# Kernel tuning notes

Measured on AMD Instinct MI355X. Metric: run time of the kernel, lower is better.

The kernel has to match this reference:

```python
import jax, jax.numpy as jnp
import numpy as np

B, NA, NB = 2, 2048, 2048
DIM_A, DIM_B = 256, 256
HEADS, DH_A, DH_B = 8, 64, 64
INNER_A, INNER_B = DH_A * HEADS, DH_B * HEADS
EPS = 1e-5


def layer_norm(x, w, b):
    m = jnp.mean(x, axis=-1, keepdims=True)
    v = jnp.mean(jnp.square(x - m), axis=-1, keepdims=True)
    return (x - m) * jax.lax.rsqrt(v + EPS) * w + b


def setup_inputs() -> dict:
    key = jax.random.key(0)
    ks = jax.random.split(key, 16)
    s = 0.02
    return {
        "feat_a": jax.random.normal(ks[0], (B, NA, DIM_A), jnp.float32),
        "feat_b": jax.random.normal(ks[1], (B, NB, DIM_B), jnp.float32),
        "mask_a_b": jax.random.bernoulli(ks[2], 0.5, (B, NA, NB)),
        # linear weights stored (in, out)
        "Wq": jax.random.normal(ks[3], (DIM_A, INNER_B), jnp.float32) * s,
        "bq": jnp.zeros((INNER_B,), jnp.float32),
        "Wk": jax.random.normal(ks[4], (DIM_B, INNER_B), jnp.float32) * s,
        "bk": jnp.zeros((INNER_B,), jnp.float32),
        "Wv": jax.random.normal(ks[5], (DIM_B, INNER_A), jnp.float32) * s,
        "bv": jnp.zeros((INNER_A,), jnp.float32),
        "Wg": jax.random.normal(ks[6], (DIM_A, INNER_A), jnp.float32) * s,
        "bg": jnp.zeros((INNER_A,), jnp.float32),
        "Wo": jax.random.normal(ks[7], (INNER_A, DIM_A), jnp.float32) * s,
        "bo": jnp.zeros((DIM_A,), jnp.float32),
        "ln_a_w": jnp.ones((DIM_A,), jnp.float32),
        "ln_a_b": jnp.zeros((DIM_A,), jnp.float32),
        "ln_b_w": jnp.ones((DIM_B,), jnp.float32),
        "ln_b_b": jnp.zeros((DIM_B,), jnp.float32),
        "qln_w": jnp.ones((INNER_B,), jnp.float32),
        "qln_b": jnp.zeros((INNER_B,), jnp.float32),
        "kln_w": jnp.ones((INNER_B,), jnp.float32),
        "kln_b": jnp.zeros((INNER_B,), jnp.float32),
    }


def reference(feat_a, feat_b, mask_a_b, Wq, bq, Wk, bk, Wv, bv, Wg, bg, Wo, bo,
              ln_a_w, ln_a_b, ln_b_w, ln_b_b, qln_w, qln_b, kln_w, kln_b):
    scale = DH_B ** -0.5
    fa = layer_norm(feat_a, ln_a_w, ln_a_b)            # (b, na, dim_a)
    fb = layer_norm(feat_b, ln_b_w, ln_b_b)            # (b, nb, dim_b)
    q = layer_norm(fa @ Wq + bq, qln_w, qln_b)         # (b, na, inner_b)
    k = layer_norm(fb @ Wk + bk, kln_w, kln_b)         # (b, nb, inner_b)
    v = fb @ Wv + bv                                   # (b, nb, inner_a)
    g = fa @ Wg + bg                                   # (b, na, inner_a)
    q = q.reshape(B, NA, HEADS, DH_B)
    k = k.reshape(B, NB, HEADS, DH_B)
    v = v.reshape(B, NB, HEADS, DH_A)
    g = g.reshape(B, NA, HEADS, DH_A)
    sim = jnp.einsum('bihd,bjhd->bhij', q, k) * scale  # (b, h, na, nb)
    neg = jnp.finfo(sim.dtype).min
    sim = jnp.where(mask_a_b[:, None, :, :], sim, neg)
    attn = jax.nn.softmax(sim, axis=-1)
    out = jnp.einsum('bhij,bjhd->bihd', attn, v)       # (b, na, h, dh_a)
    out = jax.nn.sigmoid(g) * out
    out = out.reshape(B, NA, INNER_A)
    return out @ Wo + bo                               # (b, na, dim_a)
```

## Files before the change

### kernel.cpp

```cpp
#include <hip/hip_runtime.h>
#include <hip/hip_bf16.h>

using bf16 = __hip_bfloat16;
typedef short bf16x8 __attribute__((ext_vector_type(8)));
typedef float f32x4 __attribute__((ext_vector_type(4)));
typedef unsigned short ushort8_t __attribute__((ext_vector_type(8)));
typedef unsigned long long u64;

static constexpr int NA_ = 2048, NB_ = 2048;
static constexpr int H_ = 8, DH_ = 64, INNER_ = 512;
static constexpr int MROWS = 2 * NA_;

#define MFMA32(a, b, c) __builtin_amdgcn_mfma_f32_16x16x32_bf16(a, b, c, 0, 0, 0)

#if __has_builtin(__builtin_amdgcn_exp2f)
#define EXP2(x) __builtin_amdgcn_exp2f(x)
#else
#define EXP2(x) exp2f(x)
#endif

__device__ __forceinline__ unsigned short bfbits(float x) {
  bf16 h = __float2bfloat16(x);
  return __builtin_bit_cast(unsigned short, h);
}
__device__ __forceinline__ float b2f(unsigned short u) {
  unsigned v = ((unsigned)u) << 16;
  return __builtin_bit_cast(float, v);
}

__device__ __forceinline__ unsigned pkbf(float a, float b) {
  unsigned ua = __builtin_bit_cast(unsigned, a) + 0x8000u;
  unsigned ub = __builtin_bit_cast(unsigned, b) + 0x8000u;
#if __has_builtin(__builtin_amdgcn_perm)
  return __builtin_amdgcn_perm(ub, ua, 0x07060302u);
#else
  return (ua >> 16) | (ub & 0xFFFF0000u);
#endif
}

__global__ __launch_bounds__(256) void prep_kernel(
    const float* __restrict__ fa_in, const float* __restrict__ fb_in,
    const float* __restrict__ law, const float* __restrict__ lab,
    const float* __restrict__ lbw, const float* __restrict__ lbb,
    bf16* __restrict__ fa, bf16* __restrict__ fb,
    const float* __restrict__ Wq, const float* __restrict__ Wk,
    const float* __restrict__ Wv, const float* __restrict__ Wg,
    const float* __restrict__ Wo,
    bf16* __restrict__ Wqt, bf16* __restrict__ Wkt,
    bf16* __restrict__ Wvt, bf16* __restrict__ Wgt,
    bf16* __restrict__ Woth, bf16* __restrict__ Wotl,
    const void* __restrict__ maskp, u64* __restrict__ mbits) {
  int blk = blockIdx.x;
  int t = threadIdx.x;
  if (blk < 2048) {
    int row = blk * 4 + (t >> 6);
    int lane = t & 63;
    const float *src, *w, *bb;
    bf16* dst;
    int r;
    if (row < MROWS) { src = fa_in; w = law; bb = lab; dst = fa; r = row; }
    else             { src = fb_in; w = lbw; bb = lbb; dst = fb; r = row - MROWS; }
    float4 x = *(const float4*)(src + (size_t)r * 256 + lane * 4);
    float s  = (x.x + x.y) + (x.z + x.w);
    float s2 = (x.x * x.x + x.y * x.y) + (x.z * x.z + x.w * x.w);
#pragma unroll
    for (int m = 32; m >= 1; m >>= 1) { s += __shfl_xor(s, m); s2 += __shfl_xor(s2, m); }
    float mean = s * (1.0f / 256.0f);
    float var  = s2 * (1.0f / 256.0f) - mean * mean;
    float rstd = rsqrtf(var + 1e-5f);
    float4 wv = *(const float4*)(w + lane * 4);
    float4 bv = *(const float4*)(bb + lane * 4);
    ushort4 o;
    o.x = bfbits((x.x - mean) * rstd * wv.x + bv.x);
    o.y = bfbits((x.y - mean) * rstd * wv.y + bv.y);
    o.z = bfbits((x.z - mean) * rstd * wv.z + bv.z);
    o.w = bfbits((x.w - mean) * rstd * wv.w + bv.w);
    *(ushort4*)(dst + (size_t)r * 256 + lane * 4) = o;
  } else if (blk < 4608) {
    int z = (blk - 2048) >> 9;
    int idx = ((blk - 2048) & 511) * 256 + t;
    if (z < 4) {
      const float* W = (z == 0) ? Wq : (z == 1) ? Wk : (z == 2) ? Wv : Wg;
      bf16* Wt = (z == 0) ? Wqt : (z == 1) ? Wkt : (z == 2) ? Wvt : Wgt;
      int kk = idx >> 9, n = idx & 511;
      Wt[n * 256 + kk] = __float2bfloat16(W[idx]);
    } else {
      int kk = idx >> 8, n = idx & 255;
      float w = Wo[idx];
      bf16 hi = __float2bfloat16(w);
      Woth[n * 512 + kk] = hi;
      Wotl[n * 512 + kk] = __float2bfloat16(w - __bfloat162float(hi));
    }
  } else {
    __shared__ unsigned shf[4];
    const unsigned char* mu = (const unsigned char*)maskp;
    bool nz = ((t & 3) != 0) && (mu[t] != 0);
    u64 bal = __ballot(nz);
    if ((t & 63) == 0) shf[t >> 6] = (bal != 0ull) ? 1u : 0u;
    __syncthreads();
    bool m8 = (shf[0] | shf[1] | shf[2] | shf[3]) != 0;
    int lane = t & 63, wid = t >> 6;
    int lb = blk - 4608;
    for (size_t word = (size_t)lb * 4 + wid; word < 131072; word += 8192) {
      size_t e = word * 64 + lane;
      int v = m8 ? (int)mu[e] : ((const int*)maskp)[e];
      u64 b2 = __ballot(v != 0);
      if (lane == 0) mbits[word] = b2;
    }
  }
}

__global__ __launch_bounds__(256) void gemm4_kernel(
    const bf16* __restrict__ fa, const bf16* __restrict__ fb,
    const bf16* __restrict__ Wqt, const bf16* __restrict__ Wkt,
    const bf16* __restrict__ Wgt, const bf16* __restrict__ Wvt,
    const float* __restrict__ bq, const float* __restrict__ bk,
    const float* __restrict__ bg, const float* __restrict__ bv,
    const float* __restrict__ qlw, const float* __restrict__ qlb,
    const float* __restrict__ klw, const float* __restrict__ klb,
    bf16* __restrict__ qo, bf16* __restrict__ ko,
    bf16* __restrict__ gout, bf16* __restrict__ vout) {
  __shared__ __align__(16) char sm[27648];
  int z = blockIdx.z;
  int t = threadIdx.x, wave = t >> 6, lane = t & 63;
  int lm = lane & 15, quad = lane >> 4, q8 = quad * 8;

  if (z < 2) {
    bf16* As = (bf16*)sm;
    float* Pred = (float*)(sm + 16896);
    float* MV   = (float*)(sm + 17408);
    const bf16* A    = z ? fb : fa;
    const bf16* Wt   = z ? Wkt : Wqt;
    const float* bias = z ? bk : bq;
    const float* lw  = z ? klw : qlw;
    const float* lb  = z ? klb : qlb;
    bf16* out        = z ? ko : qo;
    int m0 = blockIdx.x * 16;
#pragma unroll
    for (int i = 0; i < 2; i++) {
      int id = t + 256 * i, r = id >> 5, cg = id & 31;
      *(ushort8_t*)(&As[r * 264 + cg * 8]) =
          *(const ushort8_t*)(A + (size_t)(m0 + r) * 256 + cg * 8);
    }
    __syncthreads();
    int n0w = wave * 128;
    f32x4 acc[8] = {};
    const bf16* wrow[8];
#pragma unroll
    for (int ni = 0; ni < 8; ni++) wrow[ni] = Wt + (size_t)(n0w + ni * 16 + lm) * 256;
#pragma unroll
    for (int ks = 0; ks < 8; ks++) {
      int k0 = ks * 32;
      bf16x8 af = *(const bf16x8*)(&As[lm * 264 + k0 + q8]);
#pragma unroll
      for (int ni = 0; ni < 8; ni++) {
        bf16x8 bf_ = *(const bf16x8*)(wrow[ni] + k0 + q8);
        acc[ni] = MFMA32(af, bf_, acc[ni]);
      }
    }
    float bvv[8];
#pragma unroll
    for (int ni = 0; ni < 8; ni++) bvv[ni] = bias[n0w + ni * 16 + lm];
#pragma unroll
    for (int ni = 0; ni < 8; ni++)
#pragma unroll
      for (int r = 0; r < 4; r++) acc[ni][r] += bvv[ni];
#pragma unroll
    for (int r = 0; r < 4; r++) {
      float s = 0.f, s2 = 0.f;
#pragma unroll
      for (int ni = 0; ni < 8; ni++) { s += acc[ni][r]; s2 += acc[ni][r] * acc[ni][r]; }
#pragma unroll
      for (int m = 1; m <= 8; m <<= 1) { s += __shfl_xor(s, m); s2 += __shfl_xor(s2, m); }
      if (lm == 0) {
        int row = quad * 4 + r;
        Pred[row * 8 + wave * 2]     = s;
        Pred[row * 8 + wave * 2 + 1] = s2;
      }
    }
    __syncthreads();
    if (t < 16) {
      float s = 0.f, s2 = 0.f;
#pragma unroll
      for (int w = 0; w < 4; w++) { s += Pred[t * 8 + w * 2]; s2 += Pred[t * 8 + w * 2 + 1]; }
      float mean = s * (1.0f / 512.0f);
      float var  = s2 * (1.0f / 512.0f) - mean * mean;
      MV[t * 2]     = mean;
      MV[t * 2 + 1] = rsqrtf(var + 1e-5f);
    }
    __syncthreads();
    float lww[8], lbb_[8];
#pragma unroll
    for (int ni = 0; ni < 8; ni++) {
      lww[ni]  = lw[n0w + ni * 16 + lm];
      lbb_[ni] = lb[n0w + ni * 16 + lm];
    }
    if (z == 0) {
      const float SC = 0.125f * 1.44269504088896f;
#pragma unroll
      for (int ni = 0; ni < 8; ni++) { lww[ni] *= SC; lbb_[ni] *= SC; }
    }
#pragma unroll
    for (int r = 0; r < 4; r++) {
      int row = quad * 4 + r;
      float mean = MV[row * 2], rstd = MV[row * 2 + 1];
      size_t obase = (size_t)(m0 + row) * 512 + n0w;
#pragma unroll
      for (int ni = 0; ni < 8; ni++)
        out[obase + ni * 16 + lm] =
            __float2bfloat16((acc[ni][r] - mean) * rstd * lww[ni] + lbb_[ni]);
    }
  } else {
    bf16* As = (bf16*)sm;
    bf16* Bs = (bf16*)(sm + 18432);
    const bf16* A    = (z == 3) ? fb : fa;
    const bf16* Wt   = (z == 3) ? Wvt : Wgt;
    const float* bias = (z == 3) ? bv : bg;
    int x = blockIdx.x;
    int m0 = (x >> 3) * 128, n0 = (x & 7) * 64;
    int wm = wave * 32;
    f32x4 acc[2][4] = {};
    for (int k0 = 0; k0 < 256; k0 += 64) {
      __syncthreads();
#pragma unroll
      for (int i = 0; i < 4; i++) {
        int id = t + 256 * i, r = id >> 3, cg = id & 7;
        *(ushort8_t*)(&As[r * 72 + cg * 8]) =
            *(const ushort8_t*)(A + (size_t)(m0 + r) * 256 + k0 + cg * 8);
      }
#pragma unroll
      for (int i = 0; i < 2; i++) {
        int id = t + 256 * i, r = id >> 3, cg = id & 7;
        *(ushort8_t*)(&Bs[r * 72 + cg * 8]) =
            *(const ushort8_t*)(Wt + (size_t)(n0 + r) * 256 + k0 + cg * 8);
      }
      __syncthreads();
#pragma unroll
      for (int kk = 0; kk < 64; kk += 32) {
        bf16x8 af[2], bf_[4];
#pragma unroll
        for (int mi = 0; mi < 2; mi++)
          af[mi] = *(const bf16x8*)(&As[(wm + mi * 16 + lm) * 72 + kk + q8]);
#pragma unroll
        for (int ni = 0; ni < 4; ni++)
          bf_[ni] = *(const bf16x8*)(&Bs[(ni * 16 + lm) * 72 + kk + q8]);
#pragma unroll
        for (int mi = 0; mi < 2; mi++)
#pragma unroll
          for (int ni = 0; ni < 4; ni++)
            acc[mi][ni] = MFMA32(af[mi], bf_[ni], acc[mi][ni]);
      }
    }
    if (z == 2) {
#pragma unroll
      for (int mi = 0; mi < 2; mi++)
#pragma unroll
        for (int ni = 0; ni < 4; ni++) {
          int nn = n0 + ni * 16 + lm;
          float bvv = bias[nn];
          int mb = m0 + wm + mi * 16 + quad * 4;
#pragma unroll
          for (int r = 0; r < 4; r++)
            gout[(size_t)(mb + r) * 512 + nn] = __float2bfloat16(acc[mi][ni][r] + bvv);
        }
    } else {
      __syncthreads();
      bf16* buf = (bf16*)sm;
#pragma unroll
      for (int mi = 0; mi < 2; mi++)
#pragma unroll
        for (int ni = 0; ni < 4; ni++) {
          int d_local = ni * 16 + lm;
          float bvv = bias[n0 + d_local];
          int j_local = wm + mi * 16 + quad * 4;
#pragma unroll
          for (int r = 0; r < 4; r++)
            buf[d_local * 136 + j_local + r] = __float2bfloat16(acc[mi][ni][r] + bvv);
        }
      __syncthreads();
      int bidx2 = m0 >> 11, j0g = m0 & 2047, hh = n0 >> 6;
      int dl = t >> 2, jseg = (t & 3) * 32;
      bf16* dstrow = vout + (size_t)((bidx2 * 8 + hh) * 64 + dl) * 2048 + j0g + jseg;
#pragma unroll
      for (int c = 0; c < 4; c++)
        *(ushort8_t*)(dstrow + c * 8) = *(const ushort8_t*)(&buf[dl * 136 + jseg + c * 8]);
    }
  }
}

__global__ __launch_bounds__(512) void attn_kernel(
    const bf16* __restrict__ q, const bf16* __restrict__ k,
    const bf16* __restrict__ vt, const bf16* __restrict__ g,
    const u64* __restrict__ mbits,
    bf16* __restrict__ gh, bf16* __restrict__ gl) {
  __shared__ __align__(16) char smem[65024];
  bf16* Qs = (bf16*)smem;
  bf16* KsB = (bf16*)(smem + 9216);
  bf16* VsB = (bf16*)(smem + 27648);
  bf16* PsB = (bf16*)(smem + 46080);
  float* Om = (float*)(smem + 9216);
  float* Lbuf = (float*)(smem + 64512);

  int qt = blockIdx.x, bh = blockIdx.y;
  int bidx = bh >> 3, h = bh & 7;
  int i0 = qt * 64;
  int t = threadIdx.x, wave = t >> 6, lane = t & 63;
  int jhalf = wave >> 2, w4 = wave & 3;
  int lm = lane & 15, quad = lane >> 4, q8 = quad * 8;
  int lt = t & 255;
  int sr0 = lt >> 3, scg = (lt & 7) * 8;

  {
    int r = t >> 3, cg = t & 7;
    *(ushort8_t*)(&Qs[r * 72 + cg * 8]) =
        *(const ushort8_t*)(q + (size_t)(bidx * NA_ + i0 + r) * INNER_ + h * DH_ + cg * 8);
  }
  __syncthreads();
  bf16x8 bq0 = *(const bf16x8*)(&Qs[(w4 * 16 + lm) * 72 + q8]);
  bf16x8 bq1 = *(const bf16x8*)(&Qs[(w4 * 16 + lm) * 72 + 32 + q8]);

  bf16x8 bone;
  {
    short onev = (lm == 0) ? (short)0x3F80 : (short)0;
#pragma unroll
    for (int i = 0; i < 8; i++) bone[i] = onev;
  }

  f32x4 oacc[4] = {};
  f32x4 lacc = {};

  const bf16* kb = k + (size_t)(bidx * NB_) * INNER_ + h * DH_;
  const bf16* vb = vt + (size_t)(bh * DH_) * NB_;
  bf16* Pw = PsB + wave * (16 * 72);
  bf16* Ks = KsB + jhalf * (64 * 72);
  bf16* Vs = VsB + jhalf * (64 * 72);
  const u64* mrp = mbits + ((size_t)(bidx * NA_ + i0 + w4 * 16 + lm)) * (NB_ / 64) + jhalf * 16;

  const bf16* ksrc0 = kb + (size_t)(jhalf * 1024 + sr0) * INNER_ + scg;
  const bf16* ksrc1 = kb + (size_t)(jhalf * 1024 + sr0 + 32) * INNER_ + scg;
  const bf16* vsrc0 = vb + (size_t)sr0 * NB_ + jhalf * 1024 + scg;
  const bf16* vsrc1 = vb + (size_t)(sr0 + 32) * NB_ + jhalf * 1024 + scg;

  ushort8_t kr0, kr1, vr0, vr1;
  kr0 = *(const ushort8_t*)(ksrc0);
  kr1 = *(const ushort8_t*)(ksrc1);
  vr0 = *(const ushort8_t*)(vsrc0);
  vr1 = *(const ushort8_t*)(vsrc1);
  u64 smw = mrp[0] >> (quad * 4);

  for (int it = 0; it < 16; it++) {
    __syncthreads();
    *(ushort8_t*)(&Ks[sr0 * 72 + scg])        = kr0;
    *(ushort8_t*)(&Ks[(sr0 + 32) * 72 + scg]) = kr1;
    *(ushort8_t*)(&Vs[sr0 * 72 + scg])        = vr0;
    *(ushort8_t*)(&Vs[(sr0 + 32) * 72 + scg]) = vr1;
    __syncthreads();

    u64 nsm = smw;
    if (it < 15) {
      int joff = (it + 1) * 64;
      kr0 = *(const ushort8_t*)(ksrc0 + (size_t)joff * INNER_);
      kr1 = *(const ushort8_t*)(ksrc1 + (size_t)joff * INNER_);
      vr0 = *(const ushort8_t*)(vsrc0 + joff);
      vr1 = *(const ushort8_t*)(vsrc1 + joff);
      nsm = mrp[it + 1] >> (quad * 4);
    }

    f32x4 st[4];
#pragma unroll
    for (int nt = 0; nt < 4; nt++) {
      bf16x8 a0 = *(const bf16x8*)(&Ks[(nt * 16 + lm) * 72 + q8]);
      bf16x8 a1 = *(const bf16x8*)(&Ks[(nt * 16 + lm) * 72 + 32 + q8]);
      f32x4 a = {0.f, 0.f, 0.f, 0.f};
      a = MFMA32(a0, bq0, a);
      a = MFMA32(a1, bq1, a);
      st[nt] = a;
    }

    float pr[4][4];
#pragma unroll
    for (int nt = 0; nt < 4; nt++)
#pragma unroll
      for (int r = 0; r < 4; r++) {
        bool live = (smw >> (nt * 16 + r)) & 1ull;
        float sv = live ? st[nt][r] : -200.0f;
        pr[nt][r] = EXP2(sv);
      }

#pragma unroll
    for (int nt = 0; nt < 4; nt++) {
      uint2 pk;
      pk.x = pkbf(pr[nt][0], pr[nt][1]);
      pk.y = pkbf(pr[nt][2], pr[nt][3]);
      *(uint2*)(Pw + lm * 72 + nt * 16 + quad * 4) = pk;
    }

    bf16x8 ap0 = *(const bf16x8*)(&Pw[lm * 72 + q8]);
    bf16x8 ap1 = *(const bf16x8*)(&Pw[lm * 72 + 32 + q8]);
#pragma unroll
    for (int c = 0; c < 4; c++) {
      bf16x8 v0 = *(const bf16x8*)(&Vs[(c * 16 + lm) * 72 + q8]);
      bf16x8 v1 = *(const bf16x8*)(&Vs[(c * 16 + lm) * 72 + 32 + q8]);
      oacc[c] = MFMA32(ap0, v0, oacc[c]);
      oacc[c] = MFMA32(ap1, v1, oacc[c]);
    }
    lacc = MFMA32(ap0, bone, lacc);
    lacc = MFMA32(ap1, bone, lacc);

    smw = nsm;
  }

  __syncthreads();
  if (lm == 0) {
#pragma unroll
    for (int r = 0; r < 4; r++)
      Lbuf[jhalf * 64 + w4 * 16 + quad * 4 + r] = lacc[r];
  }
  if (jhalf == 1) {
#pragma unroll
    for (int c = 0; c < 4; c++)
#pragma unroll
      for (int r = 0; r < 4; r++)
        Om[w4 * (16 * 66) + (quad * 4 + r) * 66 + c * 16 + lm] = oacc[c][r];
  }
  __syncthreads();
  if (jhalf == 0) {
    int mrow = i0 + w4 * 16 + quad * 4;
    float inv[4];
#pragma unroll
    for (int r = 0; r < 4; r++) {
      float l = Lbuf[w4 * 16 + quad * 4 + r] + Lbuf[64 + w4 * 16 + quad * 4 + r];
      inv[r] = 1.0f / l;
    }
#pragma unroll
    for (int c = 0; c < 4; c++) {
      int col = h * DH_ + c * 16 + lm;
#pragma unroll
      for (int r = 0; r < 4; r++) {
        float o = oacc[c][r] + Om[w4 * (16 * 66) + (quad * 4 + r) * 66 + c * 16 + lm];
        size_t idx = (size_t)(bidx * NA_ + mrow + r) * INNER_ + col;
        float gv = b2f(__builtin_bit_cast(unsigned short, g[idx]));
        float sig = 1.0f / (1.0f + __expf(-gv));
        float val = o * inv[r] * sig;
        unsigned short hb = bfbits(val);
        gh[idx] = __builtin_bit_cast(bf16, hb);
        gl[idx] = __float2bfloat16(val - b2f(hb));
      }
    }
  }
}

__global__ __launch_bounds__(256) void gemm_split_kernel(
    const bf16* __restrict__ Ah, const bf16* __restrict__ Al,
    const bf16* __restrict__ Bh, const bf16* __restrict__ Bl,
    const float* __restrict__ bias, float* __restrict__ C) {
  constexpr int K = 512, N = 256;
  __shared__ __align__(16) bf16 Ash[32 * 72];
  __shared__ __align__(16) bf16 Asl[32 * 72];
  __shared__ __align__(16) bf16 Bsh[64 * 72];
  __shared__ __align__(16) bf16 Bsl[64 * 72];
  int n0 = blockIdx.x * 64, m0 = blockIdx.y * 32;
  int t = threadIdx.x, wave = t >> 6, lane = t & 63;
  int lm = lane & 15, quad = lane >> 4, q8 = quad * 8;
  int wm = (wave & 1) * 16, wn = (wave >> 1) * 32;
  f32x4 acc[2] = {};
  for (int k0 = 0; k0 < K; k0 += 64) {
    __syncthreads();
    {
      int r = t >> 3, cg = t & 7;
      size_t ga = (size_t)(m0 + r) * K + k0 + cg * 8;
      *(ushort8_t*)(&Ash[r * 72 + cg * 8]) = *(const ushort8_t*)(Ah + ga);
      *(ushort8_t*)(&Asl[r * 72 + cg * 8]) = *(const ushort8_t*)(Al + ga);
    }
#pragma unroll
    for (int i = 0; i < 2; i++) {
      int id = t + 256 * i, r = id >> 3, cg = id & 7;
      size_t gb = (size_t)(n0 + r) * K + k0 + cg * 8;
      *(ushort8_t*)(&Bsh[r * 72 + cg * 8]) = *(const ushort8_t*)(Bh + gb);
      *(ushort8_t*)(&Bsl[r * 72 + cg * 8]) = *(const ushort8_t*)(Bl + gb);
    }
    __syncthreads();
#pragma unroll
    for (int kk = 0; kk < 64; kk += 32) {
      bf16x8 ah = *(const bf16x8*)(&Ash[(wm + lm) * 72 + kk + q8]);
      bf16x8 al = *(const bf16x8*)(&Asl[(wm + lm) * 72 + kk + q8]);
#pragma unroll
      for (int ni = 0; ni < 2; ni++) {
        bf16x8 bh_ = *(const bf16x8*)(&Bsh[(wn + ni * 16 + lm) * 72 + kk + q8]);
        bf16x8 bl_ = *(const bf16x8*)(&Bsl[(wn + ni * 16 + lm) * 72 + kk + q8]);
        acc[ni] = MFMA32(ah, bh_, acc[ni]);
        acc[ni] = MFMA32(ah, bl_, acc[ni]);
        acc[ni] = MFMA32(al, bh_, acc[ni]);
      }
    }
  }
#pragma unroll
  for (int ni = 0; ni < 2; ni++) {
    int n = n0 + wn + ni * 16 + lm;
    float bvv = bias[n];
    int mb = m0 + wm + quad * 4;
#pragma unroll
    for (int r = 0; r < 4; r++) C[(size_t)(mb + r) * N + n] = acc[ni][r] + bvv;
  }
}

extern "C" void kernel_launch(void* const* d_in, const int* in_sizes, int n_in,
                              void* d_out, int out_size, void* d_ws, size_t ws_size,
                              hipStream_t stream) {
  const float* feat_a = (const float*)d_in[0];
  const float* feat_b = (const float*)d_in[1];
  const void*  mask   = d_in[2];
  const float* Wq = (const float*)d_in[3];
  const float* bq = (const float*)d_in[4];
  const float* Wk = (const float*)d_in[5];
  const float* bk = (const float*)d_in[6];
  const float* Wv = (const float*)d_in[7];
  const float* bv = (const float*)d_in[8];
  const float* Wg = (const float*)d_in[9];
  const float* bg = (const float*)d_in[10];
  const float* Wo = (const float*)d_in[11];
  const float* bo = (const float*)d_in[12];
  const float* law = (const float*)d_in[13];
  const float* lab = (const float*)d_in[14];
  const float* lbw = (const float*)d_in[15];
  const float* lbb = (const float*)d_in[16];
  const float* qlw = (const float*)d_in[17];
  const float* qlb = (const float*)d_in[18];
  const float* klw = (const float*)d_in[19];
  const float* klb = (const float*)d_in[20];

  char* ws = (char*)d_ws;
  size_t off = 0;
  auto alloc = [&](size_t bytes) -> void* {
    void* p = ws + off;
    off += (bytes + 255) & ~(size_t)255;
    return p;
  };
  bf16* fa    = (bf16*)alloc((size_t)MROWS * 256 * 2);
  bf16* fb    = (bf16*)alloc((size_t)MROWS * 256 * 2);
  bf16* Wqt   = (bf16*)alloc((size_t)131072 * 2);
  bf16* Wkt   = (bf16*)alloc((size_t)131072 * 2);
  bf16* Wvt   = (bf16*)alloc((size_t)131072 * 2);
  bf16* Wgt   = (bf16*)alloc((size_t)131072 * 2);
  bf16* Woth  = (bf16*)alloc((size_t)131072 * 2);
  bf16* Wotl  = (bf16*)alloc((size_t)131072 * 2);
  bf16* qb_   = (bf16*)alloc((size_t)MROWS * 512 * 2);
  bf16* kb_   = (bf16*)alloc((size_t)MROWS * 512 * 2);
  bf16* vtb   = (bf16*)alloc((size_t)1024 * 2048 * 2);
  bf16* gbuf  = (bf16*)alloc((size_t)MROWS * 512 * 2);
  bf16* gh    = (bf16*)alloc((size_t)MROWS * 512 * 2);
  bf16* gl    = (bf16*)alloc((size_t)MROWS * 512 * 2);
  u64*  mbits = (u64*)alloc((size_t)131072 * 8);

  prep_kernel<<<6656, 256, 0, stream>>>(
      feat_a, feat_b, law, lab, lbw, lbb, fa, fb,
      Wq, Wk, Wv, Wg, Wo, Wqt, Wkt, Wvt, Wgt, Woth, Wotl, mask, mbits);
  gemm4_kernel<<<dim3(256, 1, 4), 256, 0, stream>>>(
      fa, fb, Wqt, Wkt, Wgt, Wvt, bq, bk, bg, bv,
      qlw, qlb, klw, klb, qb_, kb_, gbuf, vtb);
  attn_kernel<<<dim3(32, 16), 512, 0, stream>>>(qb_, kb_, vtb, gbuf, mbits, gh, gl);
  gemm_split_kernel<<<dim3(4, 128), 256, 0, stream>>>(gh, gl, Woth, Wotl, bo, (float*)d_out);
}
```

Baseline: 200.6 us.

## Permute K rows in LDS so P stays in registers for PV MFMA

```diff
diff --git a/kernel.cpp b/kernel.cpp
--- a/kernel.cpp
+++ b/kernel.cpp
@@ -5,6 +5,7 @@
 typedef short bf16x8 __attribute__((ext_vector_type(8)));
 typedef float f32x4 __attribute__((ext_vector_type(4)));
 typedef unsigned short ushort8_t __attribute__((ext_vector_type(8)));
+typedef unsigned uint4_t __attribute__((ext_vector_type(4)));
 typedef unsigned long long u64;
 
 static constexpr int NA_ = 2048, NB_ = 2048;
@@ -288,18 +289,17 @@
   }
 }
 
-__global__ __launch_bounds__(512) void attn_kernel(
+__global__ __launch_bounds__(512, 6) void attn_kernel(
     const bf16* __restrict__ q, const bf16* __restrict__ k,
     const bf16* __restrict__ vt, const bf16* __restrict__ g,
     const u64* __restrict__ mbits,
     bf16* __restrict__ gh, bf16* __restrict__ gl) {
-  __shared__ __align__(16) char smem[65024];
+  __shared__ __align__(16) char smem[46592];
   bf16* Qs = (bf16*)smem;
   bf16* KsB = (bf16*)(smem + 9216);
   bf16* VsB = (bf16*)(smem + 27648);
-  bf16* PsB = (bf16*)(smem + 46080);
   float* Om = (float*)(smem + 9216);
-  float* Lbuf = (float*)(smem + 64512);
+  float* Lbuf = (float*)(smem + 46080);
 
   int qt = blockIdx.x, bh = blockIdx.y;
   int bidx = bh >> 3, h = bh & 7;
@@ -310,6 +310,12 @@
   int lt = t & 255;
   int sr0 = lt >> 3, scg = (lt & 7) * 8;
 
+  int ksrow = ((sr0 & 4) << 2) | ((sr0 & 24) >> 1) | (sr0 & 3);
+  int ksl0 = ksrow * 72 + scg;
+  int ksl1 = (ksrow + 32) * 72 + scg;
+  int vsl0 = sr0 * 72 + scg;
+  int vsl1 = (sr0 + 32) * 72 + scg;
+
   {
     int r = t >> 3, cg = t & 7;
     *(ushort8_t*)(&Qs[r * 72 + cg * 8]) =
@@ -331,7 +337,6 @@
 
   const bf16* kb = k + (size_t)(bidx * NB_) * INNER_ + h * DH_;
   const bf16* vb = vt + (size_t)(bh * DH_) * NB_;
-  bf16* Pw = PsB + wave * (16 * 72);
   bf16* Ks = KsB + jhalf * (64 * 72);
   bf16* Vs = VsB + jhalf * (64 * 72);
   const u64* mrp = mbits + ((size_t)(bidx * NA_ + i0 + w4 * 16 + lm)) * (NB_ / 64) + jhalf * 16;
@@ -346,14 +351,14 @@
   kr1 = *(const ushort8_t*)(ksrc1);
   vr0 = *(const ushort8_t*)(vsrc0);
   vr1 = *(const ushort8_t*)(vsrc1);
-  u64 smw = mrp[0] >> (quad * 4);
+  u64 smw = mrp[0] >> (quad * 8);
 
   for (int it = 0; it < 16; it++) {
     __syncthreads();
-    *(ushort8_t*)(&Ks[sr0 * 72 + scg])        = kr0;
-    *(ushort8_t*)(&Ks[(sr0 + 32) * 72 + scg]) = kr1;
-    *(ushort8_t*)(&Vs[sr0 * 72 + scg])        = vr0;
-    *(ushort8_t*)(&Vs[(sr0 + 32) * 72 + scg]) = vr1;
+    *(ushort8_t*)(&Ks[ksl0]) = kr0;
+    *(ushort8_t*)(&Ks[ksl1]) = kr1;
+    *(ushort8_t*)(&Vs[vsl0]) = vr0;
+    *(ushort8_t*)(&Vs[vsl1]) = vr1;
     __syncthreads();
 
     u64 nsm = smw;
@@ -363,7 +368,7 @@
       kr1 = *(const ushort8_t*)(ksrc1 + (size_t)joff * INNER_);
       vr0 = *(const ushort8_t*)(vsrc0 + joff);
       vr1 = *(const ushort8_t*)(vsrc1 + joff);
-      nsm = mrp[it + 1] >> (quad * 4);
+      nsm = mrp[it + 1] >> (quad * 8);
     }
 
     f32x4 st[4];
@@ -382,21 +387,24 @@
     for (int nt = 0; nt < 4; nt++)
 #pragma unroll
       for (int r = 0; r < 4; r++) {
-        bool live = (smw >> (nt * 16 + r)) & 1ull;
+        int bitix = (nt >> 1) * 32 + (nt & 1) * 4 + r;
+        bool live = (smw >> bitix) & 1ull;
         float sv = live ? st[nt][r] : -200.0f;
         pr[nt][r] = EXP2(sv);
       }
 
-#pragma unroll
-    for (int nt = 0; nt < 4; nt++) {
-      uint2 pk;
-      pk.x = pkbf(pr[nt][0], pr[nt][1]);
-      pk.y = pkbf(pr[nt][2], pr[nt][3]);
-      *(uint2*)(Pw + lm * 72 + nt * 16 + quad * 4) = pk;
-    }
-
-    bf16x8 ap0 = *(const bf16x8*)(&Pw[lm * 72 + q8]);
-    bf16x8 ap1 = *(const bf16x8*)(&Pw[lm * 72 + 32 + q8]);
+    uint4_t ua, ub;
+    ua[0] = pkbf(pr[0][0], pr[0][1]);
+    ua[1] = pkbf(pr[0][2], pr[0][3]);
+    ua[2] = pkbf(pr[1][0], pr[1][1]);
+    ua[3] = pkbf(pr[1][2], pr[1][3]);
+    ub[0] = pkbf(pr[2][0], pr[2][1]);
+    ub[1] = pkbf(pr[2][2], pr[2][3]);
+    ub[2] = pkbf(pr[3][0], pr[3][1]);
+    ub[3] = pkbf(pr[3][2], pr[3][3]);
+    bf16x8 ap0 = __builtin_bit_cast(bf16x8, ua);
+    bf16x8 ap1 = __builtin_bit_cast(bf16x8, ub);
+
 #pragma unroll
     for (int c = 0; c < 4; c++) {
       bf16x8 v0 = *(const bf16x8*)(&Vs[(c * 16 + lm) * 72 + q8]);
```

Measured after the change: 195.1 us. 1.03x faster.

## Restructure attention kernel with double-buffered shared K/V tiles and register P operand

Applied to the files above, without the earlier changes.

```diff
diff --git a/kernel.cpp b/kernel.cpp
--- a/kernel.cpp
+++ b/kernel.cpp
@@ -5,6 +5,8 @@
 typedef short bf16x8 __attribute__((ext_vector_type(8)));
 typedef float f32x4 __attribute__((ext_vector_type(4)));
 typedef unsigned short ushort8_t __attribute__((ext_vector_type(8)));
+typedef unsigned uint4_t __attribute__((ext_vector_type(4)));
+typedef unsigned uint2_t __attribute__((ext_vector_type(2)));
 typedef unsigned long long u64;
 
 static constexpr int NA_ = 2048, NB_ = 2048;
@@ -288,36 +290,53 @@
   }
 }
 
-__global__ __launch_bounds__(512) void attn_kernel(
+__global__ __launch_bounds__(512, 4) void attn_kernel(
     const bf16* __restrict__ q, const bf16* __restrict__ k,
     const bf16* __restrict__ vt, const bf16* __restrict__ g,
     const u64* __restrict__ mbits,
     bf16* __restrict__ gh, bf16* __restrict__ gl) {
-  __shared__ __align__(16) char smem[65024];
+  __shared__ __align__(16) char smem[46592];
   bf16* Qs = (bf16*)smem;
-  bf16* KsB = (bf16*)(smem + 9216);
-  bf16* VsB = (bf16*)(smem + 27648);
-  bf16* PsB = (bf16*)(smem + 46080);
+  bf16* KVB = (bf16*)(smem + 9216);
   float* Om = (float*)(smem + 9216);
-  float* Lbuf = (float*)(smem + 64512);
-
-  int qt = blockIdx.x, bh = blockIdx.y;
+  float* Lbuf = (float*)(smem + 46080);
+  constexpr int BUFE = 2 * 64 * 72;
+
+  int flat = blockIdx.y * 32 + blockIdx.x;
+  int bh = (flat & 7) * 2 + (flat >> 8);
+  int qt = (flat >> 3) & 31;
   int bidx = bh >> 3, h = bh & 7;
   int i0 = qt * 64;
   int t = threadIdx.x, wave = t >> 6, lane = t & 63;
-  int jhalf = wave >> 2, w4 = wave & 3;
+  int wj = wave >> 2, wi = wave & 3;
   int lm = lane & 15, quad = lane >> 4, q8 = quad * 8;
-  int lt = t & 255;
-  int sr0 = lt >> 3, scg = (lt & 7) * 8;
-
-  {
-    int r = t >> 3, cg = t & 7;
-    *(ushort8_t*)(&Qs[r * 72 + cg * 8]) =
-        *(const ushort8_t*)(q + (size_t)(bidx * NA_ + i0 + r) * INNER_ + h * DH_ + cg * 8);
-  }
+  int wj32 = wj * 32, wi16 = wi * 16;
+  int srow = t >> 3, scg = (t & 7) * 8;
+
+  int sg = srow & 31;
+  int ksrow = (srow & 32) + (((sg & 4) << 2) | ((sg & 24) >> 1) | (sg & 3));
+  int ksl = ksrow * 72 + scg;
+  int vsl = srow * 72 + scg;
+
+  const bf16* kb = k + (size_t)(bidx * NB_) * INNER_ + h * DH_;
+  const bf16* vb = vt + (size_t)(bh * DH_) * NB_;
+  const bf16* ksrc = kb + (size_t)srow * INNER_ + scg;
+  const bf16* vsrc = vb + (size_t)srow * NB_ + scg;
+
+  *(ushort8_t*)(&Qs[srow * 72 + scg]) =
+      *(const ushort8_t*)(q + (size_t)(bidx * NA_ + i0 + srow) * INNER_ + h * DH_ + scg);
+
+  ushort8_t kr = *(const ushort8_t*)(ksrc);
+  ushort8_t vr = *(const ushort8_t*)(vsrc);
+
   __syncthreads();
-  bf16x8 bq0 = *(const bf16x8*)(&Qs[(w4 * 16 + lm) * 72 + q8]);
-  bf16x8 bq1 = *(const bf16x8*)(&Qs[(w4 * 16 + lm) * 72 + 32 + q8]);
+  bf16x8 bq0 = *(const bf16x8*)(&Qs[(wi16 + lm) * 72 + q8]);
+  bf16x8 bq1 = *(const bf16x8*)(&Qs[(wi16 + lm) * 72 + 32 + q8]);
+
+  *(ushort8_t*)(&KVB[ksl]) = kr;
+  *(ushort8_t*)(&KVB[64 * 72 + vsl]) = vr;
+  kr = *(const ushort8_t*)(ksrc + 64 * INNER_);
+  vr = *(const ushort8_t*)(vsrc + 64);
 
   bf16x8 bone;
   {
@@ -329,124 +348,104 @@
   f32x4 oacc[4] = {};
   f32x4 lacc = {};
 
-  const bf16* kb = k + (size_t)(bidx * NB_) * INNER_ + h * DH_;
-  const bf16* vb = vt + (size_t)(bh * DH_) * NB_;
-  bf16* Pw = PsB + wave * (16 * 72);
-  bf16* Ks = KsB + jhalf * (64 * 72);
-  bf16* Vs = VsB + jhalf * (64 * 72);
-  const u64* mrp = mbits + ((size_t)(bidx * NA_ + i0 + w4 * 16 + lm)) * (NB_ / 64) + jhalf * 16;
-
-  const bf16* ksrc0 = kb + (size_t)(jhalf * 1024 + sr0) * INNER_ + scg;
-  const bf16* ksrc1 = kb + (size_t)(jhalf * 1024 + sr0 + 32) * INNER_ + scg;
-  const bf16* vsrc0 = vb + (size_t)sr0 * NB_ + jhalf * 1024 + scg;
-  const bf16* vsrc1 = vb + (size_t)(sr0 + 32) * NB_ + jhalf * 1024 + scg;
-
-  ushort8_t kr0, kr1, vr0, vr1;
-  kr0 = *(const ushort8_t*)(ksrc0);
-  kr1 = *(const ushort8_t*)(ksrc1);
-  vr0 = *(const ushort8_t*)(vsrc0);
-  vr1 = *(const ushort8_t*)(vsrc1);
-  u64 smw = mrp[0] >> (quad * 4);
-
-  for (int it = 0; it < 16; it++) {
-    __syncthreads();
-    *(ushort8_t*)(&Ks[sr0 * 72 + scg])        = kr0;
-    *(ushort8_t*)(&Ks[(sr0 + 32) * 72 + scg]) = kr1;
-    *(ushort8_t*)(&Vs[sr0 * 72 + scg])        = vr0;
-    *(ushort8_t*)(&Vs[(sr0 + 32) * 72 + scg]) = vr1;
-    __syncthreads();
-
-    u64 nsm = smw;
-    if (it < 15) {
-      int joff = (it + 1) * 64;
-      kr0 = *(const ushort8_t*)(ksrc0 + (size_t)joff * INNER_);
-      kr1 = *(const ushort8_t*)(ksrc1 + (size_t)joff * INNER_);
-      vr0 = *(const ushort8_t*)(vsrc0 + joff);
-      vr1 = *(const ushort8_t*)(vsrc1 + joff);
-      nsm = mrp[it + 1] >> (quad * 4);
-    }
-
-    f32x4 st[4];
-#pragma unroll
-    for (int nt = 0; nt < 4; nt++) {
-      bf16x8 a0 = *(const bf16x8*)(&Ks[(nt * 16 + lm) * 72 + q8]);
-      bf16x8 a1 = *(const bf16x8*)(&Ks[(nt * 16 + lm) * 72 + 32 + q8]);
-      f32x4 a = {0.f, 0.f, 0.f, 0.f};
-      a = MFMA32(a0, bq0, a);
-      a = MFMA32(a1, bq1, a);
-      st[nt] = a;
-    }
-
-    float pr[4][4];
-#pragma unroll
-    for (int nt = 0; nt < 4; nt++)
-#pragma unroll
-      for (int r = 0; r < 4; r++) {
-        bool live = (smw >> (nt * 16 + r)) & 1ull;
-        float sv = live ? st[nt][r] : -200.0f;
-        pr[nt][r] = EXP2(sv);
-      }
-
-#pragma unroll
-    for (int nt = 0; nt < 4; nt++) {
-      uint2 pk;
-      pk.x = pkbf(pr[nt][0], pr[nt][1]);
-      pk.y = pkbf(pr[nt][2], pr[nt][3]);
-      *(uint2*)(Pw + lm * 72 + nt * 16 + quad * 4) = pk;
-    }
-
-    bf16x8 ap0 = *(const bf16x8*)(&Pw[lm * 72 + q8]);
-    bf16x8 ap1 = *(const bf16x8*)(&Pw[lm * 72 + 32 + q8]);
+  const u64* mrp = mbits + (size_t)(bidx * NA_ + i0 + wi16 + lm) * (NB_ / 64);
+  int shp = wj32 + quad * 8;
+  u64 smw = mrp[0] >> shp;
+
+  __syncthreads();
+
+  for (int it = 0; it < 32; it++) {
+    bf16* Ks = KVB + (it & 1) * BUFE;
+    bf16* Vs = Ks + 64 * 72;
+    if (it < 31) {
+      bf16* Kn = KVB + ((it + 1) & 1) * BUFE;
+      *(ushort8_t*)(&Kn[ksl]) = kr;
+      *(ushort8_t*)(&Kn[64 * 72 + vsl]) = vr;
+    }
+    if (it < 30) {
+      kr = *(const ushort8_t*)(ksrc + (size_t)(it + 2) * (64 * INNER_));
+      vr = *(const ushort8_t*)(vsrc + (it + 2) * 64);
+    }
+    u64 nm = (it < 31) ? (mrp[it + 1] >> shp) : 0;
+
+    bf16x8 a00 = *(const bf16x8*)(&Ks[(wj32 + lm) * 72 + q8]);
+    bf16x8 a01 = *(const bf16x8*)(&Ks[(wj32 + lm) * 72 + 32 + q8]);
+    bf16x8 a10 = *(const bf16x8*)(&Ks[(wj32 + 16 + lm) * 72 + q8]);
+    bf16x8 a11 = *(const bf16x8*)(&Ks[(wj32 + 16 + lm) * 72 + 32 + q8]);
+    f32x4 st0 = {0.f, 0.f, 0.f, 0.f}, st1 = {0.f, 0.f, 0.f, 0.f};
+    st0 = MFMA32(a00, bq0, st0);
+    st0 = MFMA32(a01, bq1, st0);
+    st1 = MFMA32(a10, bq0, st1);
+    st1 = MFMA32(a11, bq1, st1);
+
+    float p0[4], p1[4];
+#pragma unroll
+    for (int r = 0; r < 4; r++) {
+      bool l0 = (smw >> r) & 1ull;
+      bool l1 = (smw >> (4 + r)) & 1ull;
+      p0[r] = EXP2(l0 ? st0[r] : -200.0f);
+      p1[r] = EXP2(l1 ? st1[r] : -200.0f);
+    }
+
+    uint4_t u0;
+    u0[0] = pkbf(p0[0], p0[1]);
+    u0[1] = pkbf(p0[2], p0[3]);
+    u0[2] = pkbf(p1[0], p1[1]);
+    u0[3] = pkbf(p1[2], p1[3]);
+    bf16x8 pa = __builtin_bit_cast(bf16x8, u0);
+
 #pragma unroll
     for (int c = 0; c < 4; c++) {
-      bf16x8 v0 = *(const bf16x8*)(&Vs[(c * 16 + lm) * 72 + q8]);
-      bf16x8 v1 = *(const bf16x8*)(&Vs[(c * 16 + lm) * 72 + 32 + q8]);
-      oacc[c] = MFMA32(ap0, v0, oacc[c]);
-      oacc[c] = MFMA32(ap1, v1, oacc[c]);
-    }
-    lacc = MFMA32(ap0, bone, lacc);
-    lacc = MFMA32(ap1, bone, lacc);
-
-    smw = nsm;
-  }
-
+      bf16x8 v_ = *(const bf16x8*)(&Vs[(c * 16 + lm) * 72 + wj32 + q8]);
+      oacc[c] = MFMA32(pa, v_, oacc[c]);
+    }
+    lacc = MFMA32(pa, bone, lacc);
+
+    smw = nm;
+    __syncthreads();
+  }
+
+  if (lm == 0) {
+#pragma unroll
+    for (int r = 0; r < 4; r++)
+      Lbuf[wj * 64 + wi16 + quad * 4 + r] = lacc[r];
+  }
+  if (wj == 1) {
+#pragma unroll
+    for (int c = 0; c < 4; c++)
+#pragma unroll
+      for (int r = 0; r < 4; r++)
+        Om[(wi16 + quad * 4 + r) * 66 + c * 16 + lm] = oacc[c][r];
+  }
   __syncthreads();
-  if (lm == 0) {
-#pragma unroll
-    for (int r = 0; r < 4; r++)
-      Lbuf[jhalf * 64 + w4 * 16 + quad * 4 + r] = lacc[r];
-  }
-  if (jhalf == 1) {
+  if (wj == 0) {
 #pragma unroll
     for (int c = 0; c < 4; c++)
 #pragma unroll
       for (int r = 0; r < 4; r++)
-        Om[w4 * (16 * 66) + (quad * 4 + r) * 66 + c * 16 + lm] = oacc[c][r];
+        Om[(wi16 + quad * 4 + r) * 66 + c * 16 + lm] += oacc[c][r];
   }
   __syncthreads();
-  if (jhalf == 0) {
-    int mrow = i0 + w4 * 16 + quad * 4;
-    float inv[4];
-#pragma unroll
-    for (int r = 0; r < 4; r++) {
-      float l = Lbuf[w4 * 16 + quad * 4 + r] + Lbuf[64 + w4 * 16 + quad * 4 + r];
-      inv[r] = 1.0f / l;
-    }
-#pragma unroll
-    for (int c = 0; c < 4; c++) {
-      int col = h * DH_ + c * 16 + lm;
-#pragma unroll
-      for (int r = 0; r < 4; r++) {
-        float o = oacc[c][r] + Om[w4 * (16 * 66) + (quad * 4 + r) * 66 + c * 16 + lm];
-        size_t idx = (size_t)(bidx * NA_ + mrow + r) * INNER_ + col;
-        float gv = b2f(__builtin_bit_cast(unsigned short, g[idx]));
-        float sig = 1.0f / (1.0f + __expf(-gv));
-        float val = o * inv[r] * sig;
-        unsigned short hb = bfbits(val);
-        gh[idx] = __builtin_bit_cast(bf16, hb);
-        gl[idx] = __float2bfloat16(val - b2f(hb));
-      }
-    }
+  {
+    int row = wave * 8 + (lane >> 3);
+    int col = (lane & 7) * 8;
+    float l = Lbuf[row] + Lbuf[64 + row];
+    float inv = 1.0f / l;
+    size_t idx = (size_t)(bidx * NA_ + i0 + row) * INNER_ + h * DH_ + col;
+    ushort8_t gv = *(const ushort8_t*)(g + idx);
+    ushort8_t oh, ol;
+#pragma unroll
+    for (int e = 0; e < 8; e++) {
+      float o = Om[row * 66 + col + e];
+      float gf = b2f((unsigned short)gv[e]);
+      float sig = 1.0f / (1.0f + __expf(-gf));
+      float val = o * inv * sig;
+      unsigned short hb = bfbits(val);
+      oh[e] = hb;
+      ol[e] = bfbits(val - b2f(hb));
+    }
+    *(ushort8_t*)(gh + idx) = oh;
+    *(ushort8_t*)(gl + idx) = ol;
   }
 }
 
```

After: 189.2 us. -5.7%, faster.
